# Optimization experiments

Hardware: AMD Instinct MI355X
Metric: run time of the kernel (lower is better)

## Reference

```python
import jax, jax.numpy as jnp
import numpy as np

# irreps: 128x0e + 128x1o + 128x2e -> per-irrep (mul, ir_dim)
MULS = [128, 128, 128]
IR_DIMS = [1, 3, 5]
IN_DIM = sum(m * d for m, d in zip(MULS, IR_DIMS))  # 1152
WEIGHT_NUMEL = sum(m * m for m in MULS)             # 49152
ALPHA = 128.0 ** -0.5  # path_weight, element normalization (fan-in mul = 128)
N_NODES = 100000


def setup_inputs() -> dict:
    key = jax.random.key(0)
    kx, kw = jax.random.split(key)
    x = jax.random.normal(kx, (N_NODES, IN_DIM), dtype=jnp.float32)
    w = jax.random.normal(kw, (WEIGHT_NUMEL,), dtype=jnp.float32)
    return {"x": x, "w": w}


def reference(x, w):
    # x: [B, 1152]; w: [49152] flat per-instruction blocks of shape (mul_in, mul_out)
    B = x.shape[0]
    outs = []
    x_off = 0
    w_off = 0
    for mul, d in zip(MULS, IR_DIMS):
        xb = x[:, x_off:x_off + mul * d].reshape(B, mul, d)       # [B, u, i]
        wb = w[w_off:w_off + mul * mul].reshape(mul, mul)         # [u, w]
        yb = ALPHA * jnp.einsum('uw,zui->zwi', wb, xb)            # [B, w, i]
        outs.append(yb.reshape(B, mul * d))
        x_off += mul * d
        w_off += mul * mul
    return jnp.concatenate(outs, axis=-1)  # [B, 1152]
```

## Files before the change

kernel.cpp:

```cpp
#include <hip/hip_runtime.h>
#include <stdint.h>


#define NROWS 100000
#define ROWLEN 1152

typedef __attribute__((ext_vector_type(8))) short bf16x8;
typedef __attribute__((ext_vector_type(4))) float f32x4;
typedef __attribute__((ext_vector_type(4))) ushort u16x4;

__device__ __forceinline__ ushort f2b(float f) {
  union { float f; uint32_t u; } v; v.f = f;
  uint32_t r = v.u + 0x7FFFu + ((v.u >> 16) & 1u);
  return (ushort)(r >> 16);
}


template<int D, int TM, bool G>
__device__ __forceinline__ void load_tile(const float* __restrict__ xb, int t,
                                          int tid, f32x4 (&vf)[TM / 8][D])
{
  #pragma unroll
  for (int p = 0; p < TM / 8; ++p) {
    int ch = p * 256 + tid;
    int zl = ch >> 5, cc = ch & 31;
    int z  = t * TM + zl;
    const float* src = xb + (size_t)z * ROWLEN + cc * 4 * D;
    #pragma unroll
    for (int j = 0; j < D; ++j) {
      f32x4 v = {0.f, 0.f, 0.f, 0.f};
      if (!G || z < NROWS) v = *(const f32x4*)(src + 4 * j);
      vf[p][j] = v;
    }
  }
}

template<int D, int TM>
__device__ __forceinline__ void write_tile(char* __restrict__ buf, int tid,
                                           f32x4 (&vf)[TM / 8][D])
{
  #pragma unroll
  for (int p = 0; p < TM / 8; ++p) {
    int ch = p * 256 + tid;
    int zl = ch >> 5, cc = ch & 31;
    #pragma unroll
    for (int i = 0; i < D; ++i) {
      int m = i * TM + zl;
      u16x4 pk;
      #pragma unroll
      for (int u = 0; u < 4; ++u) {
        int e = i + D * u;
        pk[u] = f2b(vf[p][e >> 2][e & 3]);
      }
      int byte = m * 256 + ((((cc >> 1) ^ (m & 7)) << 4) | ((cc & 1) << 3));
      *(u16x4*)(buf + byte) = pk;
    }
  }
}

template<bool G, int D, int TM, int MTILES>
__device__ __forceinline__ void store_tile(float* __restrict__ ob, int z0,
                                           int lane, int nbase,
                                           f32x4 (&acc)[MTILES][2])
{
  const int rbase = ((lane >> 4) & 3) << 2;
  #pragma unroll
  for (int mt = 0; mt < MTILES; ++mt) {
    #pragma unroll
    for (int r = 0; r < 4; ++r) {
      int m  = mt * 16 + rbase + r;
      int i  = m / TM, zl = m % TM;
      int z  = z0 + zl;
      if (G && z >= NROWS) continue;
      float* orow = ob + (size_t)z * ROWLEN + i;
      orow[(size_t)nbase * D]        = acc[mt][0][r];
      orow[(size_t)(nbase + 16) * D] = acc[mt][1][r];
    }
  }
}

template<int D, int TM, bool GUARD, int NWGS>
__device__ __forceinline__ void linpath(const float* __restrict__ xb,
                                        const float* __restrict__ wb,
                                        float* __restrict__ ob,
                                        int wgid, char* lds)
{
  constexpr int MT     = TM * D;
  constexpr int MTILES = MT / 16;
  constexpr int PT     = TM / 8;
  constexpr int NTILES = (NROWS + TM - 1) / TM;
  constexpr int BUFB   = MT * 256;
  constexpr float ALPHA = 0.088388347648318447f;

  const int tid   = threadIdx.x;
  const int lane  = tid & 63;
  const int wv    = tid >> 6;
  const int l15   = lane & 15;
  const int kr    = ((lane >> 4) & 3) << 3;
  const int nbase = (wv << 5) + l15;

  bf16x8 bfr[2][4];
  #pragma unroll
  for (int nt = 0; nt < 2; ++nt)
    #pragma unroll
    for (int ks = 0; ks < 4; ++ks)
      #pragma unroll
      for (int j = 0; j < 8; ++j)
        bfr[nt][ks][j] =
            (short)f2b(wb[(ks * 32 + kr + j) * 128 + nbase + nt * 16] * ALPHA);

  char* buf0 = lds;
  char* buf1 = lds + BUFB;

  int t0 = wgid;
  {
    f32x4 vf[PT][D];
    if (GUARD && t0 == NTILES - 1) load_tile<D, TM, true>(xb, t0, tid, vf);
    else                           load_tile<D, TM, false>(xb, t0, tid, vf);
    write_tile<D, TM>(buf0, tid, vf);
  }
  __syncthreads();

  int cur = 0;
  for (int t = t0; t < NTILES; t += NWGS) {
    char* bc = cur ? buf1 : buf0;
    char* bn = cur ? buf0 : buf1;
    const int tn = t + NWGS;
    const bool have = tn < NTILES;

    f32x4 vf[PT][D];
    if (have) {
      if (GUARD && tn == NTILES - 1) load_tile<D, TM, true>(xb, tn, tid, vf);
      else                           load_tile<D, TM, false>(xb, tn, tid, vf);
    }

    f32x4 acc[MTILES][2];
    #pragma unroll
    for (int mt = 0; mt < MTILES; ++mt) {
      acc[mt][0] = f32x4{0.f, 0.f, 0.f, 0.f};
      acc[mt][1] = f32x4{0.f, 0.f, 0.f, 0.f};
    }
    #pragma unroll
    for (int ks = 0; ks < 4; ++ks) {
      const int chunkbase = ks * 4 + ((lane >> 4) & 3);
      #pragma unroll
      for (int mt = 0; mt < MTILES; ++mt) {
        int m = (mt << 4) + l15;
        int byte = m * 256 + ((chunkbase ^ (m & 7)) << 4);
        bf16x8 a = *(const bf16x8*)(bc + byte);
        acc[mt][0] = __builtin_amdgcn_mfma_f32_16x16x32_bf16(a, bfr[0][ks], acc[mt][0], 0, 0, 0);
        acc[mt][1] = __builtin_amdgcn_mfma_f32_16x16x32_bf16(a, bfr[1][ks], acc[mt][1], 0, 0, 0);
      }
    }

    if (have) write_tile<D, TM>(bn, tid, vf);

    if (GUARD && t == NTILES - 1)
      store_tile<true, D, TM, MTILES>(ob, t * TM, lane, nbase, acc);
    else
      store_tile<false, D, TM, MTILES>(ob, t * TM, lane, nbase, acc);

    __syncthreads();
    cur ^= 1;
  }
}

constexpr int NW1 = 84;
constexpr int NW3 = 254;
constexpr int NW5 = 430;

__global__ __launch_bounds__(256, 3)
void linear_irreps_kernel(const float* __restrict__ x, const float* __restrict__ w,
                          float* __restrict__ out)
{
  extern __shared__ __align__(16) char lds[];
  int wg = blockIdx.x;
  if (wg < NW1) {
    linpath<1, 64, true,  NW1>(x,       w,         out,       wg,             lds);
  } else if (wg < NW1 + NW3) {
    linpath<3, 16, false, NW3>(x + 128, w + 16384, out + 128, wg - NW1,       lds);
  } else {
    linpath<5, 16, false, NW5>(x + 512, w + 32768, out + 512, wg - NW1 - NW3, lds);
  }
}

extern "C" void kernel_launch(void* const* d_in, const int* in_sizes, int n_in,
                              void* d_out, int out_size, void* d_ws, size_t ws_size,
                              hipStream_t stream) {
  const float* x = (const float*)d_in[0];
  const float* w = (const float*)d_in[1];
  float* out = (float*)d_out;
  (void)in_sizes; (void)n_in; (void)out_size; (void)d_ws; (void)ws_size;
  dim3 grid(NW1 + NW3 + NW5);
  dim3 block(256);
  hipLaunchKernelGGL(linear_irreps_kernel, grid, block, 40960, stream, x, w, out);
}
```

Measured before the change: 206.1 us.

## Stage D=3 and D=5 outputs through LDS for coalesced vector stores

Measured after the change: 501.9 us. 2.44x slower.

```diff
diff --git a/kernel.cpp b/kernel.cpp
--- a/kernel.cpp
+++ b/kernel.cpp
@@ -14,7 +14,6 @@
   uint32_t r = v.u + 0x7FFFu + ((v.u >> 16) & 1u);
   return (ushort)(r >> 16);
 }
-
 
 template<int D, int TM, bool G>
 __device__ __forceinline__ void load_tile(const float* __restrict__ xb, int t,
@@ -59,9 +58,9 @@
 }
 
 template<bool G, int D, int TM, int MTILES>
-__device__ __forceinline__ void store_tile(float* __restrict__ ob, int z0,
-                                           int lane, int nbase,
-                                           f32x4 (&acc)[MTILES][2])
+__device__ __forceinline__ void store_direct(float* __restrict__ ob, int z0,
+                                             int lane, int nbase,
+                                             f32x4 (&acc)[MTILES][2])
 {
   const int rbase = ((lane >> 4) & 3) << 2;
   #pragma unroll
@@ -79,7 +78,82 @@
   }
 }
 
-template<int D, int TM, bool GUARD, int NWGS>
+__device__ __forceinline__ char* row_base3(char* lds, char* bcp, int zl) {
+  return (zl < 10) ? (lds + 24576 + zl * 1536) : (bcp + (zl - 10) * 1536);
+}
+
+template<int MTILES>
+__device__ __forceinline__ void stage_out3(char* lds, char* bcp, int lane,
+                                           int nbase, f32x4 (&acc)[MTILES][2])
+{
+  const int rbase = ((lane >> 4) & 3) << 2;
+  #pragma unroll
+  for (int mt = 0; mt < MTILES; ++mt) {
+    #pragma unroll
+    for (int nt = 0; nt < 2; ++nt) {
+      const int col = (nbase + nt * 16) * 3 + mt;
+      #pragma unroll
+      for (int r = 0; r < 4; ++r) {
+        const int zl = rbase + r;
+        char* base = row_base3(lds, bcp, zl);
+        int byte = ((((col >> 2) ^ (zl & 7)) << 4) | ((col & 3) << 2));
+        *(float*)(base + byte) = acc[mt][nt][r];
+      }
+    }
+  }
+}
+
+__device__ __forceinline__ void store_out3(char* lds, char* bcp,
+                                           float* __restrict__ ob, int z0,
+                                           int tid)
+{
+  #pragma unroll
+  for (int p = 0; p < 6; ++p) {
+    int e   = p * 256 + tid;
+    int zl  = e / 96;
+    int c16 = e - zl * 96;
+    char* base = row_base3(lds, bcp, zl);
+    f32x4 v = *(const f32x4*)(base + ((c16 ^ (zl & 7)) << 4));
+    *(f32x4*)(ob + (size_t)(z0 + zl) * ROWLEN + c16 * 4) = v;
+  }
+}
+
+template<int H, int MTILES>
+__device__ __forceinline__ void stage_half5(char* bc, int lane, int nbase,
+                                            f32x4 (&acc)[MTILES][2])
+{
+  const int rbase = ((lane >> 4) & 3) << 2;
+  if ((rbase >> 3) != H) return;
+  #pragma unroll
+  for (int mt = 0; mt < MTILES; ++mt) {
+    #pragma unroll
+    for (int nt = 0; nt < 2; ++nt) {
+      const int col = (nbase + nt * 16) * 5 + mt;
+      #pragma unroll
+      for (int r = 0; r < 4; ++r) {
+        const int zr = (rbase + r) & 7;
+        int byte = zr * 2560 + ((((col >> 2) ^ zr) << 4) | ((col & 3) << 2));
+        *(float*)(bc + byte) = acc[mt][nt][r];
+      }
+    }
+  }
+}
+
+template<int H>
+__device__ __forceinline__ void store_half5(char* bc, float* __restrict__ ob,
+                                            int z0, int tid)
+{
+  #pragma unroll
+  for (int p = 0; p < 5; ++p) {
+    int e   = p * 256 + tid;
+    int zr  = e / 160;
+    int c16 = e - zr * 160;
+    f32x4 v = *(const f32x4*)(bc + zr * 2560 + ((c16 ^ zr) << 4));
+    *(f32x4*)(ob + (size_t)(z0 + H * 8 + zr) * ROWLEN + c16 * 4) = v;
+  }
+}
+
+template<int D, int TM, bool GUARD, int STAGE, int NWGS>
 __device__ __forceinline__ void linpath(const float* __restrict__ xb,
                                         const float* __restrict__ wb,
                                         float* __restrict__ ob,
@@ -153,14 +227,30 @@
       }
     }
 
-    if (have) write_tile<D, TM>(bn, tid, vf);
-
-    if (GUARD && t == NTILES - 1)
-      store_tile<true, D, TM, MTILES>(ob, t * TM, lane, nbase, acc);
-    else
-      store_tile<false, D, TM, MTILES>(ob, t * TM, lane, nbase, acc);
-
-    __syncthreads();
+    if (STAGE == 1) {
+      __syncthreads();
+      stage_out3<MTILES>(lds, bc, lane, nbase, acc);
+      if (have) write_tile<D, TM>(bn, tid, vf);
+      __syncthreads();
+      store_out3(lds, bc, ob, t * TM, tid);
+    } else if (STAGE == 2) {
+      __syncthreads();
+      stage_half5<0, MTILES>(bc, lane, nbase, acc);
+      if (have) write_tile<D, TM>(bn, tid, vf);
+      __syncthreads();
+      store_half5<0>(bc, ob, t * TM, tid);
+      __syncthreads();
+      stage_half5<1, MTILES>(bc, lane, nbase, acc);
+      __syncthreads();
+      store_half5<1>(bc, ob, t * TM, tid);
+    } else {
+      if (have) write_tile<D, TM>(bn, tid, vf);
+      if (GUARD && t == NTILES - 1)
+        store_direct<true, D, TM, MTILES>(ob, t * TM, lane, nbase, acc);
+      else
+        store_direct<false, D, TM, MTILES>(ob, t * TM, lane, nbase, acc);
+      __syncthreads();
+    }
     cur ^= 1;
   }
 }
@@ -176,11 +266,11 @@
   extern __shared__ __align__(16) char lds[];
   int wg = blockIdx.x;
   if (wg < NW1) {
-    linpath<1, 64, true,  NW1>(x,       w,         out,       wg,             lds);
+    linpath<1, 64, true,  0, NW1>(x,       w,         out,       wg,             lds);
   } else if (wg < NW1 + NW3) {
-    linpath<3, 16, false, NW3>(x + 128, w + 16384, out + 128, wg - NW1,       lds);
+    linpath<3, 16, false, 1, NW3>(x + 128, w + 16384, out + 128, wg - NW1,       lds);
   } else {
-    linpath<5, 16, false, NW5>(x + 512, w + 32768, out + 512, wg - NW1 - NW3, lds);
+    linpath<5, 16, false, 2, NW5>(x + 512, w + 32768, out + 512, wg - NW1 - NW3, lds);
   }
 }
 
```
